# Optimization experiments

Measured on AMD Instinct MI355X. Metric: run time of the kernel, lower is better.

## Reference

```python
import jax, jax.numpy as jnp
import numpy as np
import math

ALGEBRA_DIM = 32

def _hadamard(n):
    H = np.array([[1.0]], dtype=np.float32)
    while H.shape[0] < n:
        H = np.block([[H, H], [H, -H]])
    return H

# Sylvester-ordered Hadamard matrix, normalized: equals the butterfly FHT with /sqrt(N)
H32 = jnp.asarray(_hadamard(ALGEBRA_DIM) / math.sqrt(ALGEBRA_DIM), dtype=jnp.float32)

def quantize_ternary(w):
    # BitNet-b1.58 style absmean ternary quantization with straight-through estimator
    scale = jnp.mean(jnp.abs(w)) + 1e-8
    w_q = jnp.clip(jnp.round(w / scale), -1.0, 1.0) * scale
    return w + jax.lax.stop_gradient(w_q - w)

def setup_inputs() -> dict:
    key = jax.random.key(0)
    k1, k2, k3 = jax.random.split(key, 3)
    B, T = 4, 2048
    in_o = out_o = 128  # in_features = out_features = 4096
    x = jax.random.normal(k1, (B, T, ALGEBRA_DIM * in_o), dtype=jnp.float32)
    weight = jax.random.uniform(k2, (ALGEBRA_DIM, out_o, in_o), dtype=jnp.float32) * 2.0 - 1.0
    alpha = jnp.ones((ALGEBRA_DIM, in_o), dtype=jnp.float32)
    beta_init = math.sqrt(3.0 / (2.0 * in_o))
    beta = jnp.ones((ALGEBRA_DIM, out_o), dtype=jnp.float32) * beta_init
    return {"x": x, "weight": weight, "alpha": alpha, "beta": beta}

def reference(x, weight, alpha, beta):
    B, T, D = x.shape
    G = ALGEBRA_DIM
    in_o = D // G
    w_q = quantize_ternary(weight)                      # [G, out_o, in_o]
    xp = x.reshape(B, T, G, in_o) * alpha               # [B,T,G,in_o]
    # FHT over algebra dim G (Sylvester WHT, /sqrt(G) folded into H32)
    xm = jnp.einsum('btgi,gh->bthi', xp, H32)           # [B,T,G,in_o]
    # grouped ternary matmul: btgi,gio->btgo with w_q transposed
    yp = jnp.einsum('bthi,hoi->btho', xm, w_q)          # [B,T,G,out_o]
    ym = jnp.einsum('btho,hg->btgo', yp, H32)           # FHT over algebra dim again
    y = ym * beta                                       # [B,T,G,out_o]
    return y.reshape(B, T, -1)
```

## Files before the change

### kernel.cpp

```cpp
#include <hip/hip_runtime.h>
#include <cstdint>
#include <cstddef>

#define TM 8
#define IP 136
#define SLAB (TM * IP)

__device__ __forceinline__ unsigned short f2bf(float f) {
  union { float f; unsigned int u; } c; c.f = f;
  unsigned int u = c.u;
  return (unsigned short)((u + 0x7FFFu + ((u >> 16) & 1u)) >> 16);
}
__device__ __forceinline__ float bf2f(unsigned short h) {
  union { unsigned int u; float f; } c; c.u = ((unsigned int)h) << 16; return c.f;
}

__device__ __forceinline__ void fht32(float* v) {
  #pragma unroll
  for (int s = 1; s < 32; s <<= 1) {
    #pragma unroll
    for (int a = 0; a < 32; ++a) {
      if ((a & s) == 0) {
        float u0 = v[a], u1 = v[a + s];
        v[a] = u0 + u1;
        v[a + s] = u0 - u1;
      }
    }
  }
}

typedef __attribute__((ext_vector_type(8))) short bf16x8;
typedef __attribute__((ext_vector_type(4))) float f32x4;

__global__ void kred1(const float* __restrict__ w, double* __restrict__ partials) {
  const int tid = threadIdx.x;
  const int base = blockIdx.x * 8192 + tid;
  double s = 0.0;
  #pragma unroll
  for (int j = 0; j < 32; ++j) s += (double)fabsf(w[base + j * 256]);
  #pragma unroll
  for (int off = 32; off > 0; off >>= 1) s += __shfl_down(s, off, 64);
  __shared__ double sh[4];
  if ((tid & 63) == 0) sh[tid >> 6] = s;
  __syncthreads();
  if (tid == 0) partials[blockIdx.x] = sh[0] + sh[1] + sh[2] + sh[3];
}

__global__ void kprep(const float* __restrict__ w, const double* __restrict__ partials,
                      float* __restrict__ scale_out, unsigned short* __restrict__ wqt) {
  const int tid = threadIdx.x;
  __shared__ float s_sc;
  if (tid < 64) {
    double s = partials[tid];
    #pragma unroll
    for (int off = 32; off > 0; off >>= 1) s += __shfl_down(s, off, 64);
    if (tid == 0) s_sc = (float)(s / 524288.0) + 1e-8f;
  }
  __syncthreads();
  const float sc = s_sc;
  if (blockIdx.x == 0 && tid == 0) scale_out[0] = sc;
  const int cid = blockIdx.x * 256 + tid;
  const int lane = cid & 63, ks = (cid >> 6) & 3, nt = (cid >> 8) & 7, h = cid >> 11;
  const int m = lane & 15, quad = lane >> 4;
  const float* src = w + h * 16384 + (nt * 16 + m) * 128 + ks * 32 + quad * 8;
  bf16x8 vv;
  #pragma unroll
  for (int j = 0; j < 8; ++j) {
    float q = rintf(src[j] / sc);
    q = fminf(1.f, fmaxf(-1.f, q));
    vv[j] = (short)f2bf(q);
  }
  *(bf16x8*)(wqt + (size_t)cid * 8) = vv;
}

__global__ __launch_bounds__(512, 4) void had_main(
    const float* __restrict__ x,
    const unsigned short* __restrict__ wqt,
    const float* __restrict__ alpha,
    const float* __restrict__ beta,
    const float* __restrict__ scale_p,
    float* __restrict__ y) {
  extern __shared__ unsigned short lds[];
  const int tid = threadIdx.x;
  const long tok0 = (long)blockIdx.x * TM;
  const int i0 = tid & 127;
  const int tq = tid >> 7;

  {
    float av[32];
    #pragma unroll
    for (int g = 0; g < 32; ++g) av[g] = alpha[g * 128 + i0];
    #pragma unroll
    for (int p = 0; p < 2; ++p) {
      const int t = p * 4 + tq;
      const float* xrow = x + (size_t)(tok0 + t) * 4096 + i0;
      float v[32];
      #pragma unroll
      for (int g = 0; g < 32; ++g) v[g] = xrow[(size_t)g * 128] * av[g];
      fht32(v);
      #pragma unroll
      for (int h = 0; h < 32; ++h) lds[(h * TM + t) * IP + i0] = f2bf(v[h]);
    }
  }
  __syncthreads();

  {
    const int wave = tid >> 6;
    const int lane = tid & 63;
    const int m = lane & 15;
    const int quad = lane >> 4;
    for (int hh = 0; hh < 4; ++hh) {
      const int h = wave + hh * 8;
      unsigned short* slab = lds + h * SLAB;
      bf16x8 afr[4];
      #pragma unroll
      for (int ks = 0; ks < 4; ++ks)
        afr[ks] = *(const bf16x8*)(slab + (m & 7) * IP + ks * 32 + quad * 8);
      const unsigned short* wh = wqt + ((size_t)h * 8) * 2048;
      #pragma unroll
      for (int nt = 0; nt < 8; ++nt) {
        f32x4 acc = {0.f, 0.f, 0.f, 0.f};
        #pragma unroll
        for (int ks = 0; ks < 4; ++ks) {
          bf16x8 bfr = *(const bf16x8*)(wh + (size_t)(nt * 4 + ks) * 512 + lane * 8);
          acc = __builtin_amdgcn_mfma_f32_16x16x32_bf16(afr[ks], bfr, acc, 0, 0, 0);
        }
        if (quad < 2) {
          #pragma unroll
          for (int r = 0; r < 4; ++r)
            slab[(quad * 4 + r) * IP + nt * 16 + m] = f2bf(acc[r]);
        }
      }
    }
  }
  __syncthreads();

  {
    const float sc32 = scale_p[0] * (1.0f / 32.0f);
    float cf[32];
    #pragma unroll
    for (int g = 0; g < 32; ++g) cf[g] = beta[g * 128 + i0] * sc32;
    #pragma unroll
    for (int p = 0; p < 2; ++p) {
      const int t = p * 4 + tq;
      float v[32];
      #pragma unroll
      for (int h = 0; h < 32; ++h) v[h] = bf2f(lds[(h * TM + t) * IP + i0]);
      fht32(v);
      float* yrow = y + (size_t)(tok0 + t) * 4096 + i0;
      #pragma unroll
      for (int g = 0; g < 32; ++g) yrow[(size_t)g * 128] = v[g] * cf[g];
    }
  }
}

extern "C" void kernel_launch(void* const* d_in, const int* in_sizes, int n_in,
                              void* d_out, int out_size, void* d_ws, size_t ws_size,
                              hipStream_t stream) {
  (void)in_sizes; (void)n_in; (void)out_size; (void)ws_size;
  const float* x     = (const float*)d_in[0];
  const float* w     = (const float*)d_in[1];
  const float* alpha = (const float*)d_in[2];
  const float* beta  = (const float*)d_in[3];
  float* y = (float*)d_out;

  char* ws = (char*)d_ws;
  unsigned short* wqt = (unsigned short*)(ws);
  float* scale     = (float*)(ws + 1048576);
  double* partials = (double*)(ws + 1048584);

  (void)hipFuncSetAttribute(reinterpret_cast<const void*>(had_main),
                            hipFuncAttributeMaxDynamicSharedMemorySize, 69632);

  hipLaunchKernelGGL(kred1,    dim3(64),   dim3(256), 0,     stream, w, partials);
  hipLaunchKernelGGL(kprep,    dim3(256),  dim3(256), 0,     stream, w, partials, scale, wqt);
  hipLaunchKernelGGL(had_main, dim3(1024), dim3(512), 69632, stream, x, wqt, alpha, beta, scale, y);
}
```

Measured before the change: 279.3 us.

## Prefetch weight fragments, batch x loads for two tokens, widen reduction grid

The main kernel now loads both token rows of x before doing any FHT, so twice as many global loads are in flight at once, and alpha is applied on the fly instead of being held in registers. The MFMA loop now double-buffers the B fragments from global memory, issuing the next tile's loads before the current MFMAs. The abs-sum reduction moves from 64 blocks to 256, and the prep kernel sums four partials per thread. These changes raise memory-level parallelism at the cost of more registers per thread, which could reduce occupancy under the 512x4 launch bounds.

New measurement: 273.4 us. 2.1% less time.

```diff
diff --git a/kernel.cpp b/kernel.cpp
--- a/kernel.cpp
+++ b/kernel.cpp
@@ -34,10 +34,10 @@
 
 __global__ void kred1(const float* __restrict__ w, double* __restrict__ partials) {
   const int tid = threadIdx.x;
-  const int base = blockIdx.x * 8192 + tid;
+  const int base = blockIdx.x * 2048 + tid;
   double s = 0.0;
   #pragma unroll
-  for (int j = 0; j < 32; ++j) s += (double)fabsf(w[base + j * 256]);
+  for (int j = 0; j < 8; ++j) s += (double)fabsf(w[base + j * 256]);
   #pragma unroll
   for (int off = 32; off > 0; off >>= 1) s += __shfl_down(s, off, 64);
   __shared__ double sh[4];
@@ -51,7 +51,7 @@
   const int tid = threadIdx.x;
   __shared__ float s_sc;
   if (tid < 64) {
-    double s = partials[tid];
+    double s = partials[tid] + partials[tid + 64] + partials[tid + 128] + partials[tid + 192];
     #pragma unroll
     for (int off = 32; off > 0; off >>= 1) s += __shfl_down(s, off, 64);
     if (tid == 0) s_sc = (float)(s / 524288.0) + 1e-8f;
@@ -87,20 +87,24 @@
   const int tq = tid >> 7;
 
   {
-    float av[32];
+    const float* xrowA = x + (size_t)(tok0 + tq) * 4096 + i0;
+    const float* xrowB = x + (size_t)(tok0 + tq + 4) * 4096 + i0;
+    float va[32], vb[32];
     #pragma unroll
-    for (int g = 0; g < 32; ++g) av[g] = alpha[g * 128 + i0];
+    for (int g = 0; g < 32; ++g) va[g] = xrowA[(size_t)g * 128];
     #pragma unroll
-    for (int p = 0; p < 2; ++p) {
-      const int t = p * 4 + tq;
-      const float* xrow = x + (size_t)(tok0 + t) * 4096 + i0;
-      float v[32];
-      #pragma unroll
-      for (int g = 0; g < 32; ++g) v[g] = xrow[(size_t)g * 128] * av[g];
-      fht32(v);
-      #pragma unroll
-      for (int h = 0; h < 32; ++h) lds[(h * TM + t) * IP + i0] = f2bf(v[h]);
+    for (int g = 0; g < 32; ++g) vb[g] = xrowB[(size_t)g * 128];
+    #pragma unroll
+    for (int g = 0; g < 32; ++g) {
+      const float a = alpha[g * 128 + i0];
+      va[g] *= a; vb[g] *= a;
     }
+    fht32(va);
+    #pragma unroll
+    for (int h = 0; h < 32; ++h) lds[(h * TM + tq) * IP + i0] = f2bf(va[h]);
+    fht32(vb);
+    #pragma unroll
+    for (int h = 0; h < 32; ++h) lds[(h * TM + tq + 4) * IP + i0] = f2bf(vb[h]);
   }
   __syncthreads();
 
@@ -109,6 +113,7 @@
     const int lane = tid & 63;
     const int m = lane & 15;
     const int quad = lane >> 4;
+    #pragma unroll
     for (int hh = 0; hh < 4; ++hh) {
       const int h = wave + hh * 8;
       unsigned short* slab = lds + h * SLAB;
@@ -116,20 +121,28 @@
       #pragma unroll
       for (int ks = 0; ks < 4; ++ks)
         afr[ks] = *(const bf16x8*)(slab + (m & 7) * IP + ks * 32 + quad * 8);
-      const unsigned short* wh = wqt + ((size_t)h * 8) * 2048;
+      const unsigned short* wh = wqt + (size_t)h * 16384 + (size_t)lane * 8;
+      bf16x8 cur[4], nxt[4];
+      #pragma unroll
+      for (int ks = 0; ks < 4; ++ks) cur[ks] = *(const bf16x8*)(wh + ks * 512);
       #pragma unroll
       for (int nt = 0; nt < 8; ++nt) {
+        if (nt < 7) {
+          #pragma unroll
+          for (int ks = 0; ks < 4; ++ks)
+            nxt[ks] = *(const bf16x8*)(wh + (size_t)((nt + 1) * 4 + ks) * 512);
+        }
         f32x4 acc = {0.f, 0.f, 0.f, 0.f};
         #pragma unroll
-        for (int ks = 0; ks < 4; ++ks) {
-          bf16x8 bfr = *(const bf16x8*)(wh + (size_t)(nt * 4 + ks) * 512 + lane * 8);
-          acc = __builtin_amdgcn_mfma_f32_16x16x32_bf16(afr[ks], bfr, acc, 0, 0, 0);
-        }
+        for (int ks = 0; ks < 4; ++ks)
+          acc = __builtin_amdgcn_mfma_f32_16x16x32_bf16(afr[ks], cur[ks], acc, 0, 0, 0);
         if (quad < 2) {
           #pragma unroll
           for (int r = 0; r < 4; ++r)
             slab[(quad * 4 + r) * IP + nt * 16 + m] = f2bf(acc[r]);
         }
+        #pragma unroll
+        for (int ks = 0; ks < 4; ++ks) cur[ks] = nxt[ks];
       }
     }
   }
@@ -142,7 +155,7 @@
     for (int g = 0; g < 32; ++g) cf[g] = beta[g * 128 + i0] * sc32;
     #pragma unroll
     for (int p = 0; p < 2; ++p) {
-      const int t = p * 4 + tq;
+      const int t = tq + p * 4;
       float v[32];
       #pragma unroll
       for (int h = 0; h < 32; ++h) v[h] = bf2f(lds[(h * TM + t) * IP + i0]);
@@ -172,7 +185,7 @@
   (void)hipFuncSetAttribute(reinterpret_cast<const void*>(had_main),
                             hipFuncAttributeMaxDynamicSharedMemorySize, 69632);
 
-  hipLaunchKernelGGL(kred1,    dim3(64),   dim3(256), 0,     stream, w, partials);
+  hipLaunchKernelGGL(kred1,    dim3(256),  dim3(256), 0,     stream, w, partials);
   hipLaunchKernelGGL(kprep,    dim3(256),  dim3(256), 0,     stream, w, partials, scale, wqt);
   hipLaunchKernelGGL(had_main, dim3(1024), dim3(512), 69632, stream, x, wqt, alpha, beta, scale, y);
 }
```
